# Kernel optimization log

Hardware: AMD Instinct MI355X
Metric: run time of the kernel (lower is better)

Reference implementation:

```python
import jax, jax.numpy as jnp
import numpy as np

B, N, G, NG_MAX, D = 16, 16384, 128, 128, 256


def setup_inputs() -> dict:
    key = jax.random.key(0)
    k_feat, k_perm = jax.random.split(key)
    block_features = jax.random.normal(k_feat, (B, G, NG_MAX, D), dtype=jnp.float32)
    # Per-sample random partition of N tokens into G blocks of NG_MAX tokens each.
    perms = jax.vmap(lambda k: jax.random.permutation(k, N))(jax.random.split(k_perm, B))  # [B, N]
    block_of_token = perms // NG_MAX  # [B, N] in [0, G)
    block_onehot = jax.nn.one_hot(block_of_token, G, dtype=jnp.float32)  # [B, N, G]
    return {"block_features": block_features, "block_onehot": block_onehot, "N": N}


def reference(block_features, block_onehot, N):
    # block_features: [B, G, Ng_max, D]; block_onehot: [B, N, G]
    # Original TF loop: for each block g, for each sample, the k-th token n with
    # onehot[b,n,g] > 0 (in increasing n) receives block_features[b, g, k].
    # Later blocks overwrite earlier ones; uncovered tokens stay zero.
    Bb, Gg, ng_max, Dd = block_features.shape
    mask = block_onehot > 0                                   # [B, N, G]
    rank = jnp.cumsum(mask.astype(jnp.int32), axis=1) - 1     # per-block rank of each token
    # last block g (overwrite semantics) claiming each token
    g_idx = Gg - 1 - jnp.argmax(mask[:, :, ::-1], axis=-1)    # [B, N]
    valid = mask.any(axis=-1)                                 # [B, N]
    rank_sel = jnp.take_along_axis(rank, g_idx[..., None], axis=-1)[..., 0]
    rank_sel = jnp.clip(rank_sel, 0, ng_max - 1)
    flat_feat = block_features.reshape(Bb, Gg * ng_max, Dd)   # [B, G*Ng_max, D]
    flat_idx = g_idx * ng_max + rank_sel                      # [B, N]
    out = jnp.take_along_axis(flat_feat, flat_idx[..., None], axis=1)  # [B, N, D]
    return jnp.where(valid[..., None], out, jnp.zeros((), block_features.dtype))
```

## Files before the change

### kernel.cpp

```cpp
#include <hip/hip_runtime.h>
#include <stdint.h>

#define BB     16
#define NTOK   16384
#define GG     128
#define NGMAX  128
#define DD     256
#define NCHUNK (NTOK / 64)

typedef unsigned short     u16;
typedef unsigned int       u32;
typedef unsigned long long u64;


__global__ __launch_bounds__(256) void k_lastg(const float* __restrict__ onehot,
                                               u16* __restrict__ pack) {
    int tid   = threadIdx.x;
    int tn    = blockIdx.x * 32 + (tid >> 3);
    int inner = tid & 7;
    const float* base = onehot + (size_t)tn * GG;

    int best = -1;
#pragma unroll
    for (int j = 0; j < 4; ++j) {
        int e = inner * 4 + j * 32;
        int4 v = *reinterpret_cast<const int4*>(base + e);
        if (v.x > 0) best = e + 0;
        if (v.y > 0) best = e + 1;
        if (v.z > 0) best = e + 2;
        if (v.w > 0) best = e + 3;
    }
#pragma unroll
    for (int o = 1; o < 8; o <<= 1) {
        int other = __shfl_xor(best, o);
        best = max(best, other);
    }
    if (inner == 0) pack[tn] = (best < 0) ? (u16)0xFF00 : (u16)(best << 8);
}

__global__ __launch_bounds__(256) void k_rank64(u16* __restrict__ pack,
                                                u32* __restrict__ hist) {
    int lane  = threadIdx.x & 63;
    int wid   = threadIdx.x >> 6;
    int chunk = blockIdx.x * 4 + wid;
    int b     = chunk >> 8;
    int cb    = chunk & (NCHUNK - 1);
    int token = chunk * 64 + lane;

    unsigned g = pack[token] >> 8;

    u64 plane[8];
#pragma unroll
    for (int bit = 0; bit < 8; ++bit)
        plane[bit] = __ballot((g >> bit) & 1u);

    u64 same = ~0ull;
#pragma unroll
    for (int bit = 0; bit < 8; ++bit)
        same &= ((g >> bit) & 1u) ? plane[bit] : ~plane[bit];
    u64 below = ((u64)1 << lane) - 1;
    unsigned rank = (unsigned)__popcll(same & below);
    pack[token] = (u16)((g << 8) | rank);

#pragma unroll
    for (int h = 0; h < 2; ++h) {
        unsigned tg = (unsigned)lane + h * 64;
        u64 m = ~0ull;
#pragma unroll
        for (int bit = 0; bit < 8; ++bit)
            m &= ((tg >> bit) & 1u) ? plane[bit] : ~plane[bit];
        hist[((size_t)(b * GG + tg)) * NCHUNK + cb] = (u32)__popcll(m);
    }
}

__global__ __launch_bounds__(64) void k_scan(u32* __restrict__ hist) {
    int pair = blockIdx.x;
    int lane = threadIdx.x;
    u32* row = hist + (size_t)pair * NCHUNK;

    uint4 v = *reinterpret_cast<uint4*>(row + lane * 4);
    u32 s0 = v.x, s1 = s0 + v.y, s2 = s1 + v.z, s3 = s2 + v.w;
    u32 tot = s3, inc = tot;
#pragma unroll
    for (int o = 1; o < 64; o <<= 1) {
        u32 t = __shfl_up(inc, o);
        if (lane >= o) inc += t;
    }
    u32 excl = inc - tot;
    uint4 w;
    w.x = excl;
    w.y = excl + s0;
    w.z = excl + s1;
    w.w = excl + s2;
    *reinterpret_cast<uint4*>(row + lane * 4) = w;
}

__global__ __launch_bounds__(256) void k_gather(const float* __restrict__ feat,
                                                const u16* __restrict__ pack,
                                                const u32* __restrict__ hist,
                                                float* __restrict__ out) {
    int tid   = threadIdx.x;
    int token = blockIdx.x * 16 + (tid >> 4);
    int inner = tid & 15;
    int b     = token >> 14;
    int n     = token & (NTOK - 1);

    unsigned p = pack[token];
    unsigned g = p >> 8;
    unsigned r = p & 0xFFu;

    float4 vals[4];
    if (g < GG) {
        u32 k = r + hist[((size_t)(b * GG + g)) * NCHUNK + (n >> 6)];
        if (k > NGMAX - 1) k = NGMAX - 1;
        const float* src = feat + (((size_t)(b * GG + g)) * NGMAX + k) * DD;
#pragma unroll
        for (int j = 0; j < 4; ++j)
            vals[j] = *reinterpret_cast<const float4*>(src + inner * 4 + j * 64);
    } else {
#pragma unroll
        for (int j = 0; j < 4; ++j) vals[j] = make_float4(0.f, 0.f, 0.f, 0.f);
    }
    float* dst = out + (size_t)token * DD;
#pragma unroll
    for (int j = 0; j < 4; ++j)
        *reinterpret_cast<float4*>(dst + inner * 4 + j * 64) = vals[j];
}

extern "C" void kernel_launch(void* const* d_in, const int* in_sizes, int n_in,
                              void* d_out, int out_size, void* d_ws, size_t ws_size,
                              hipStream_t stream) {
    const float* feat   = (const float*)d_in[0];
    const float* onehot = (const float*)d_in[1];
    float*       out    = (float*)d_out;

    u16* pack = (u16*)d_ws;
    u32* hist = (u32*)((char*)d_ws + (size_t)BB * NTOK * 2);

    k_lastg <<<BB * NTOK / 32,   256, 0, stream>>>(onehot, pack);
    k_rank64<<<BB * NCHUNK / 4,  256, 0, stream>>>(pack, hist);
    k_scan  <<<BB * GG,          64,  0, stream>>>(hist);
    k_gather<<<BB * NTOK / 16,   256, 0, stream>>>(feat, pack, hist, out);
}
```

Baseline: 136.2 us.

## Fuse last-block detection with chunk ranking and use nontemporal loads/stores

Merges the last-block argmax kernel and the per-chunk rank/histogram kernel into one kernel. Each block handles one 64-token chunk and passes block ids through shared memory, which removes one launch and a round trip of the pack array through global memory. Also switches the one-hot reads and the gather loads and stores to nontemporal builtins to cut cache pollution on streaming traffic. In exchange, only one of four waves does the ballot work after the barrier, and each thread now reads 32 contiguous floats instead of interleaved segments.

```diff
diff --git a/kernel.cpp b/kernel.cpp
--- a/kernel.cpp
+++ b/kernel.cpp
@@ -11,65 +11,65 @@
 typedef unsigned short     u16;
 typedef unsigned int       u32;
 typedef unsigned long long u64;
+typedef uint8_t            u8;
+
+typedef int   __attribute__((ext_vector_type(4))) i4;
+typedef float __attribute__((ext_vector_type(4))) f4;
 
 
-__global__ __launch_bounds__(256) void k_lastg(const float* __restrict__ onehot,
-                                               u16* __restrict__ pack) {
+__global__ __launch_bounds__(256) void k_stage1(const float* __restrict__ onehot,
+                                                u16* __restrict__ pack,
+                                                u32* __restrict__ hist) {
+    __shared__ u8 gsh[64];
     int tid   = threadIdx.x;
-    int tn    = blockIdx.x * 32 + (tid >> 3);
-    int inner = tid & 7;
-    const float* base = onehot + (size_t)tn * GG;
+    int chunk = blockIdx.x;
+    int tok   = tid >> 2;
+    int part  = tid & 3;
+    const float* base = onehot + ((size_t)chunk * 64 + tok) * GG;
 
     int best = -1;
 #pragma unroll
-    for (int j = 0; j < 4; ++j) {
-        int e = inner * 4 + j * 32;
-        int4 v = *reinterpret_cast<const int4*>(base + e);
+    for (int j = 0; j < 8; ++j) {
+        int e = part * 32 + j * 4;
+        i4 v = __builtin_nontemporal_load(reinterpret_cast<const i4*>(base + e));
         if (v.x > 0) best = e + 0;
         if (v.y > 0) best = e + 1;
         if (v.z > 0) best = e + 2;
         if (v.w > 0) best = e + 3;
     }
-#pragma unroll
-    for (int o = 1; o < 8; o <<= 1) {
-        int other = __shfl_xor(best, o);
-        best = max(best, other);
-    }
-    if (inner == 0) pack[tn] = (best < 0) ? (u16)0xFF00 : (u16)(best << 8);
-}
+    best = max(best, __shfl_xor(best, 1));
+    best = max(best, __shfl_xor(best, 2));
+    if (part == 0) gsh[tok] = (best < 0) ? (u8)255 : (u8)best;
+    __syncthreads();
 
-__global__ __launch_bounds__(256) void k_rank64(u16* __restrict__ pack,
-                                                u32* __restrict__ hist) {
-    int lane  = threadIdx.x & 63;
-    int wid   = threadIdx.x >> 6;
-    int chunk = blockIdx.x * 4 + wid;
-    int b     = chunk >> 8;
-    int cb    = chunk & (NCHUNK - 1);
-    int token = chunk * 64 + lane;
+    if (tid < 64) {
+        int lane = tid;
+        unsigned g = gsh[lane];
 
-    unsigned g = pack[token] >> 8;
-
-    u64 plane[8];
-#pragma unroll
-    for (int bit = 0; bit < 8; ++bit)
-        plane[bit] = __ballot((g >> bit) & 1u);
-
-    u64 same = ~0ull;
-#pragma unroll
-    for (int bit = 0; bit < 8; ++bit)
-        same &= ((g >> bit) & 1u) ? plane[bit] : ~plane[bit];
-    u64 below = ((u64)1 << lane) - 1;
-    unsigned rank = (unsigned)__popcll(same & below);
-    pack[token] = (u16)((g << 8) | rank);
-
-#pragma unroll
-    for (int h = 0; h < 2; ++h) {
-        unsigned tg = (unsigned)lane + h * 64;
-        u64 m = ~0ull;
+        u64 plane[8];
 #pragma unroll
         for (int bit = 0; bit < 8; ++bit)
-            m &= ((tg >> bit) & 1u) ? plane[bit] : ~plane[bit];
-        hist[((size_t)(b * GG + tg)) * NCHUNK + cb] = (u32)__popcll(m);
+            plane[bit] = __ballot((g >> bit) & 1u);
+
+        u64 same = ~0ull;
+#pragma unroll
+        for (int bit = 0; bit < 8; ++bit)
+            same &= ((g >> bit) & 1u) ? plane[bit] : ~plane[bit];
+        u64 below = ((u64)1 << lane) - 1;
+        unsigned rank = (unsigned)__popcll(same & below);
+        pack[chunk * 64 + lane] = (u16)((g << 8) | rank);
+
+        int b  = chunk >> 8;
+        int cb = chunk & (NCHUNK - 1);
+#pragma unroll
+        for (int h = 0; h < 2; ++h) {
+            unsigned tg = (unsigned)lane + h * 64;
+            u64 m = ~0ull;
+#pragma unroll
+            for (int bit = 0; bit < 8; ++bit)
+                m &= ((tg >> bit) & 1u) ? plane[bit] : ~plane[bit];
+            hist[((size_t)(b * GG + tg)) * NCHUNK + cb] = (u32)__popcll(m);
+        }
     }
 }
 
@@ -109,22 +109,24 @@
     unsigned g = p >> 8;
     unsigned r = p & 0xFFu;
 
-    float4 vals[4];
+    f4 vals[4];
     if (g < GG) {
         u32 k = r + hist[((size_t)(b * GG + g)) * NCHUNK + (n >> 6)];
         if (k > NGMAX - 1) k = NGMAX - 1;
         const float* src = feat + (((size_t)(b * GG + g)) * NGMAX + k) * DD;
 #pragma unroll
         for (int j = 0; j < 4; ++j)
-            vals[j] = *reinterpret_cast<const float4*>(src + inner * 4 + j * 64);
+            vals[j] = __builtin_nontemporal_load(
+                reinterpret_cast<const f4*>(src + inner * 4 + j * 64));
     } else {
 #pragma unroll
-        for (int j = 0; j < 4; ++j) vals[j] = make_float4(0.f, 0.f, 0.f, 0.f);
+        for (int j = 0; j < 4; ++j) vals[j] = (f4){0.f, 0.f, 0.f, 0.f};
     }
     float* dst = out + (size_t)token * DD;
 #pragma unroll
     for (int j = 0; j < 4; ++j)
-        *reinterpret_cast<float4*>(dst + inner * 4 + j * 64) = vals[j];
+        __builtin_nontemporal_store(vals[j],
+            reinterpret_cast<f4*>(dst + inner * 4 + j * 64));
 }
 
 extern "C" void kernel_launch(void* const* d_in, const int* in_sizes, int n_in,
@@ -137,8 +139,7 @@
     u16* pack = (u16*)d_ws;
     u32* hist = (u32*)((char*)d_ws + (size_t)BB * NTOK * 2);
 
-    k_lastg <<<BB * NTOK / 32,   256, 0, stream>>>(onehot, pack);
-    k_rank64<<<BB * NCHUNK / 4,  256, 0, stream>>>(pack, hist);
-    k_scan  <<<BB * GG,          64,  0, stream>>>(hist);
-    k_gather<<<BB * NTOK / 16,   256, 0, stream>>>(feat, pack, hist, out);
+    k_stage1<<<BB * NCHUNK,     256, 0, stream>>>(onehot, pack, hist);
+    k_scan  <<<BB * GG,         64,  0, stream>>>(hist);
+    k_gather<<<BB * NTOK / 16,  256, 0, stream>>>(feat, pack, hist, out);
 }
```

After: 161.7 us. 1.19x slower.
